# Performance work log

Measured on AMD Instinct MI355X. Metric: run time of the kernel, lower is better.

Reference implementation:

```python
import jax, jax.numpy as jnp
import numpy as np

B, Q, K, H = 4, 512, 512, 256

def setup_inputs() -> dict:
    key = jax.random.key(0)
    ks = jax.random.split(key, 6)
    scale = 1.0 / np.sqrt(H)
    return {
        "queries": jax.random.normal(ks[0], (B, Q, H), dtype=jnp.float32),
        "keys": jax.random.normal(ks[1], (B, K, H), dtype=jnp.float32),
        "values": jax.random.normal(ks[2], (B, K, H), dtype=jnp.float32),
        "W_q": jax.random.normal(ks[3], (H, H), dtype=jnp.float32) * scale,
        "W_k": jax.random.normal(ks[4], (H, H), dtype=jnp.float32) * scale,
        "w_v": jax.random.normal(ks[5], (H,), dtype=jnp.float32) * scale,
    }

def reference(queries, keys, values, W_q, W_k, w_v):
    # Linear (no bias): x @ W.T, matching torch nn.Linear convention
    q = jnp.einsum('bqh,oh->bqo', queries, W_q)      # [B,Q,H]
    k = jnp.einsum('bkh,oh->bko', keys, W_k)          # [B,K,H]
    # broadcast add -> tanh -> linear reduce to scores [B,Q,K]
    features = jnp.tanh(q[:, :, None, :] + k[:, None, :, :])  # [B,Q,K,H]
    scores = jnp.einsum('bqkh,h->bqk', features, w_v)          # [B,Q,K]
    attn = jax.nn.softmax(scores, axis=-1)                     # [B,Q,K]
    # dropout p=0 (eval) -> identity
    return jnp.einsum('bqk,bkd->bqd', attn, values)            # [B,Q,Dv]
```

## Files before the change

kernel.cpp:

```cpp
#include <hip/hip_runtime.h>
#include <hip/hip_bf16.h>
#include <math.h>


#define B_ 4
#define Q_ 512
#define K_ 512
#define H_ 256

#define QE_ELEMS (B_ * Q_ * H_)
#define KE_ELEMS (B_ * H_ * K_)
#define HALF_ELEMS (QE_ELEMS + KE_ELEMS)

static constexpr float CEXP = 2.8853900817779268f;
static constexpr float LOG2E = 1.4426950408889634f;

__global__ __launch_bounds__(256) void proj_partial(
    const float* __restrict__ queries, const float* __restrict__ keys,
    const float* __restrict__ Wq, const float* __restrict__ Wk,
    float* __restrict__ ws)
{
    const int bid = blockIdx.x;
    const float* A; const float* S; float* Cp; int ldc;
    if (bid < 256) {
        int dhalf = bid & 1;
        int tile = bid >> 1;
        int mt = tile >> 2, nt = tile & 3;
        A = queries + (mt * 64) * H_ + dhalf * 128;
        S = Wq + (nt * 64) * H_ + dhalf * 128;
        Cp = ws + (long)dhalf * HALF_ELEMS + (mt * 64) * H_ + nt * 64;
        ldc = H_;
    } else {
        int id = bid - 256;
        int dhalf = id & 1;
        int tile = id >> 1;
        int b = tile >> 5, mt = (tile >> 3) & 3, nt = tile & 7;
        A = Wk + (mt * 64) * H_ + dhalf * 128;
        S = keys + ((long)b * K_ + nt * 64) * H_ + dhalf * 128;
        Cp = ws + (long)dhalf * HALF_ELEMS + QE_ELEMS +
             ((long)b * H_ + mt * 64) * K_ + nt * 64;
        ldc = K_;
    }

    __shared__ float As[2][16][68];
    __shared__ float Ss[2][16][68];

    const int tid = threadIdx.x;
    const int tx = tid & 15;
    const int ty = tid >> 4;
    const int ldr = tid >> 2;
    const int ldd = (tid & 3) * 4;

    const float* GA = A + ldr * H_ + ldd;
    const float* GS = S + ldr * H_ + ldd;

    float4 av = *(const float4*)GA;
    float4 sv = *(const float4*)GS;
    As[0][ldd + 0][ldr] = av.x; As[0][ldd + 1][ldr] = av.y;
    As[0][ldd + 2][ldr] = av.z; As[0][ldd + 3][ldr] = av.w;
    Ss[0][ldd + 0][ldr] = sv.x; Ss[0][ldd + 1][ldr] = sv.y;
    Ss[0][ldd + 2][ldr] = sv.z; Ss[0][ldd + 3][ldr] = sv.w;

    float acc[4][4] = {};

#pragma unroll
    for (int c = 0; c < 8; ++c) {
        const int cur = c & 1;
        if (c < 7) {
            av = *(const float4*)(GA + (c + 1) * 16);
            sv = *(const float4*)(GS + (c + 1) * 16);
        }
        __syncthreads();
#pragma unroll
        for (int dd = 0; dd < 16; ++dd) {
            float4 a4 = *(const float4*)&As[cur][dd][ty * 4];
            float4 b4 = *(const float4*)&Ss[cur][dd][tx * 4];
            float am[4] = {a4.x, a4.y, a4.z, a4.w};
            float bn[4] = {b4.x, b4.y, b4.z, b4.w};
#pragma unroll
            for (int i = 0; i < 4; ++i)
#pragma unroll
                for (int j = 0; j < 4; ++j)
                    acc[i][j] = fmaf(am[i], bn[j], acc[i][j]);
        }
        if (c < 7) {
            const int nxt = cur ^ 1;
            As[nxt][ldd + 0][ldr] = av.x; As[nxt][ldd + 1][ldr] = av.y;
            As[nxt][ldd + 2][ldr] = av.z; As[nxt][ldd + 3][ldr] = av.w;
            Ss[nxt][ldd + 0][ldr] = sv.x; Ss[nxt][ldd + 1][ldr] = sv.y;
            Ss[nxt][ldd + 2][ldr] = sv.z; Ss[nxt][ldd + 3][ldr] = sv.w;
        }
    }

#pragma unroll
    for (int i = 0; i < 4; ++i) {
        float4 o = {acc[i][0], acc[i][1], acc[i][2], acc[i][3]};
        *(float4*)&Cp[(ty * 4 + i) * ldc + tx * 4] = o;
    }
}

__global__ __launch_bounds__(256) void exp_combine(float* __restrict__ ws)
{
    const int i = blockIdx.x * 256 + threadIdx.x;
    float4* w4 = (float4*)ws;
    float4 a = w4[i];
    float4 b = w4[i + HALF_ELEMS / 4];
    float4 o;
    o.x = __builtin_amdgcn_exp2f(CEXP * (a.x + b.x));
    o.y = __builtin_amdgcn_exp2f(CEXP * (a.y + b.y));
    o.z = __builtin_amdgcn_exp2f(CEXP * (a.z + b.z));
    o.w = __builtin_amdgcn_exp2f(CEXP * (a.w + b.w));
    w4[i] = o;
}

__global__ __launch_bounds__(1024, 8) void attn_fused(
    const float* __restrict__ qe, const float* __restrict__ ke,
    const float* __restrict__ values, const float* __restrict__ wv,
    float* __restrict__ out)
{
    const int b = blockIdx.y;
    const int q0 = blockIdx.x * 4;
    const int t = threadIdx.x;

    __shared__ __align__(16) float smem[4 * H_ + H_ + 4 * K_ + 4 * K_];
    float* sQ  = smem;
    float* wvs = smem + 4 * H_;
    float* sS  = smem + 5 * H_;
    float* sP  = smem + 5 * H_ + 4 * K_;

    sQ[t & 1023] = qe[((long)(b * Q_ + q0 + (t >> 8))) * H_ + (t & 255)];
    if (t < H_) wvs[t] = wv[t];
    __syncthreads();

    {
        const int k = t & 511;
        const int hh = t >> 9;
        const float* keb = ke + ((long)b * H_ + hh * 128) * K_ + k;

        float n0 = keb[0 * K_], n1 = keb[1 * K_], n2 = keb[2 * K_], n3 = keb[3 * K_];
        float acc[4] = {0.f, 0.f, 0.f, 0.f};

#pragma unroll 2
        for (int hl = 0; hl < 128; hl += 4) {
            float k0 = n0, k1 = n1, k2 = n2, k3 = n3;
            if (hl < 124) {
                const float* p = keb + (hl + 4) * K_;
                n0 = p[0]; n1 = p[K_]; n2 = p[2 * K_]; n3 = p[3 * K_];
            }
            const int h = hh * 128 + hl;
            float4 w4 = *(const float4*)&wvs[h];
#pragma unroll
            for (int q = 0; q < 4; ++q) {
                float4 e = *(const float4*)&sQ[q * H_ + h];
                float t0 = fmaf(e.x, k0, 1.0f);
                float t1 = fmaf(e.y, k1, 1.0f);
                float t2 = fmaf(e.z, k2, 1.0f);
                float t3 = fmaf(e.w, k3, 1.0f);
                float d01 = t0 * t1, d23 = t2 * t3;
                float n01 = fmaf(w4.x, t1, w4.y * t0);
                float n23 = fmaf(w4.z, t3, w4.w * t2);
                float num = fmaf(n01, d23, n23 * d01);
                acc[q] = fmaf(num, __builtin_amdgcn_rcpf(d01 * d23), acc[q]);
            }
        }

        if (hh == 1) {
#pragma unroll
            for (int q = 0; q < 4; ++q) sP[q * K_ + k] = acc[q];
        }
        __syncthreads();
        if (hh == 0) {
#pragma unroll
            for (int q = 0; q < 4; ++q)
                sS[q * K_ + k] = -2.0f * (acc[q] + sP[q * K_ + k]);
        }
    }
    __syncthreads();

    if (t < 256) {
        const int lane = t & 63;
        const int q = t >> 6;
        float sv[8];
        float m = -INFINITY;
#pragma unroll
        for (int j = 0; j < 8; ++j) {
            sv[j] = sS[q * K_ + lane + 64 * j];
            m = fmaxf(m, sv[j]);
        }
#pragma unroll
        for (int off = 32; off >= 1; off >>= 1) m = fmaxf(m, __shfl_xor(m, off));
        float sum = 0.f;
#pragma unroll
        for (int j = 0; j < 8; ++j) {
            sv[j] = __builtin_amdgcn_exp2f((sv[j] - m) * LOG2E);
            sum += sv[j];
        }
#pragma unroll
        for (int off = 32; off >= 1; off >>= 1) sum += __shfl_xor(sum, off);
        float rs = 1.0f / sum;
#pragma unroll
        for (int j = 0; j < 8; ++j) sS[q * K_ + lane + 64 * j] = sv[j] * rs;
    }
    __syncthreads();

    {
        const int lane = t & 63;
        const int h4 = lane * 4;
        const int q = (t >> 6) & 3;
        const int kq = t >> 8;
        const float* vb = values + (long)b * K_ * H_ + h4;
        const float* sSq = sS + q * K_;
        float4 acc = {0.f, 0.f, 0.f, 0.f};
        const int kbeg = kq * 128;
        for (int k = kbeg; k < kbeg + 128; k += 4) {
            float4 a = *(const float4*)&sSq[k];
            float4 v0 = *(const float4*)&vb[(k + 0) * H_];
            float4 v1 = *(const float4*)&vb[(k + 1) * H_];
            float4 v2 = *(const float4*)&vb[(k + 2) * H_];
            float4 v3 = *(const float4*)&vb[(k + 3) * H_];
            acc.x = fmaf(a.x, v0.x, fmaf(a.y, v1.x, fmaf(a.z, v2.x, fmaf(a.w, v3.x, acc.x))));
            acc.y = fmaf(a.x, v0.y, fmaf(a.y, v1.y, fmaf(a.z, v2.y, fmaf(a.w, v3.y, acc.y))));
            acc.z = fmaf(a.x, v0.z, fmaf(a.y, v1.z, fmaf(a.z, v2.z, fmaf(a.w, v3.z, acc.z))));
            acc.w = fmaf(a.x, v0.w, fmaf(a.y, v1.w, fmaf(a.z, v2.w, fmaf(a.w, v3.w, acc.w))));
        }
        __syncthreads();
        float4* sRed = (float4*)sS;
        if (kq) sRed[(kq - 1) * 256 + q * 64 + lane] = acc;
        __syncthreads();
        if (kq == 0) {
            float4 p1 = sRed[q * 64 + lane];
            float4 p2 = sRed[256 + q * 64 + lane];
            float4 p3 = sRed[512 + q * 64 + lane];
            acc.x += p1.x + p2.x + p3.x;
            acc.y += p1.y + p2.y + p3.y;
            acc.z += p1.z + p2.z + p3.z;
            acc.w += p1.w + p2.w + p3.w;
            *(float4*)&out[((long)(b * Q_ + q0 + q)) * H_ + h4] = acc;
        }
    }
}

extern "C" void kernel_launch(void* const* d_in, const int* in_sizes, int n_in,
                              void* d_out, int out_size, void* d_ws, size_t ws_size,
                              hipStream_t stream) {
    const float* queries = (const float*)d_in[0];
    const float* keys    = (const float*)d_in[1];
    const float* values  = (const float*)d_in[2];
    const float* Wq      = (const float*)d_in[3];
    const float* Wk      = (const float*)d_in[4];
    const float* wv      = (const float*)d_in[5];
    float* out = (float*)d_out;

    float* ws = (float*)d_ws;
    float* qe = ws;
    float* ke = ws + QE_ELEMS;

    proj_partial<<<512, 256, 0, stream>>>(queries, keys, Wq, Wk, ws);
    exp_combine<<<HALF_ELEMS / 1024, 256, 0, stream>>>(ws);
    attn_fused<<<dim3(Q_ / 4, B_), 1024, 0, stream>>>(qe, ke, values, wv, out);
}
```

Baseline: 137.5 us.

## Fuse projection, exp and attention into one persistent kernel with grid barrier

Merges the three launches into a single 512-block kernel. Each block first computes one projection tile, with two 256-thread teams splitting the reduction dimension and combining through LDS before applying the exp, then all blocks meet at an atomic grid barrier before the attention phase. This removes two kernel launches and the partial-sum round trip through global memory, and remaps attention blocks so batches follow XCD assignment. The trade-offs are that half the threads sit idle during the GEMM phase, and the grid barrier relies on all 512 blocks being co-resident, which would deadlock otherwise. It also adds a memset launch, double-buffers the key prefetch and unrolls the values loop.

New measurement: 318.1 us. +131.4%, slower.

```diff
diff --git a/kernel.cpp b/kernel.cpp
--- a/kernel.cpp
+++ b/kernel.cpp
@@ -7,162 +7,216 @@
 #define Q_ 512
 #define K_ 512
 #define H_ 256
-
 #define QE_ELEMS (B_ * Q_ * H_)
 #define KE_ELEMS (B_ * H_ * K_)
-#define HALF_ELEMS (QE_ELEMS + KE_ELEMS)
 
 static constexpr float CEXP = 2.8853900817779268f;
 static constexpr float LOG2E = 1.4426950408889634f;
 
-__global__ __launch_bounds__(256) void proj_partial(
+union Arena {
+    struct {
+        float As[2][2][16][68];
+        float Ss[2][2][16][68];
+    } ga;
+    struct {
+        float sQ[4 * H_];
+        float wvs[H_];
+        float sS[4 * K_];
+        float sP[4 * K_];
+    } at;
+};
+
+__device__ inline void grid_barrier(unsigned* ctr, unsigned expected) {
+    __syncthreads();
+    if (threadIdx.x == 0) {
+        __threadfence();
+        __hip_atomic_fetch_add(ctr, 1u, __ATOMIC_RELEASE,
+                               __HIP_MEMORY_SCOPE_AGENT);
+        while (__hip_atomic_load(ctr, __ATOMIC_ACQUIRE,
+                                 __HIP_MEMORY_SCOPE_AGENT) < expected)
+            __builtin_amdgcn_s_sleep(2);
+    }
+    __syncthreads();
+}
+
+__global__ __launch_bounds__(1024, 8) void fused_all(
     const float* __restrict__ queries, const float* __restrict__ keys,
-    const float* __restrict__ Wq, const float* __restrict__ Wk,
-    float* __restrict__ ws)
+    const float* __restrict__ values, const float* __restrict__ Wq,
+    const float* __restrict__ Wk, const float* __restrict__ wv,
+    float* __restrict__ ws, float* __restrict__ out,
+    unsigned* __restrict__ ctr)
 {
+    __shared__ Arena u;
     const int bid = blockIdx.x;
-    const float* A; const float* S; float* Cp; int ldc;
+    const int t = threadIdx.x;
+    float* qe = ws;
+    float* ke = ws + QE_ELEMS;
+
     if (bid < 256) {
-        int dhalf = bid & 1;
-        int tile = bid >> 1;
-        int mt = tile >> 2, nt = tile & 3;
-        A = queries + (mt * 64) * H_ + dhalf * 128;
-        S = Wq + (nt * 64) * H_ + dhalf * 128;
-        Cp = ws + (long)dhalf * HALF_ELEMS + (mt * 64) * H_ + nt * 64;
-        ldc = H_;
-    } else {
-        int id = bid - 256;
-        int dhalf = id & 1;
-        int tile = id >> 1;
-        int b = tile >> 5, mt = (tile >> 3) & 3, nt = tile & 7;
-        A = Wk + (mt * 64) * H_ + dhalf * 128;
-        S = keys + ((long)b * K_ + nt * 64) * H_ + dhalf * 128;
-        Cp = ws + (long)dhalf * HALF_ELEMS + QE_ELEMS +
-             ((long)b * H_ + mt * 64) * K_ + nt * 64;
-        ldc = K_;
-    }
-
-    __shared__ float As[2][16][68];
-    __shared__ float Ss[2][16][68];
-
-    const int tid = threadIdx.x;
-    const int tx = tid & 15;
-    const int ty = tid >> 4;
-    const int ldr = tid >> 2;
-    const int ldd = (tid & 3) * 4;
-
-    const float* GA = A + ldr * H_ + ldd;
-    const float* GS = S + ldr * H_ + ldd;
-
-    float4 av = *(const float4*)GA;
-    float4 sv = *(const float4*)GS;
-    As[0][ldd + 0][ldr] = av.x; As[0][ldd + 1][ldr] = av.y;
-    As[0][ldd + 2][ldr] = av.z; As[0][ldd + 3][ldr] = av.w;
-    Ss[0][ldd + 0][ldr] = sv.x; Ss[0][ldd + 1][ldr] = sv.y;
-    Ss[0][ldd + 2][ldr] = sv.z; Ss[0][ldd + 3][ldr] = sv.w;
-
-    float acc[4][4] = {};
-
-#pragma unroll
-    for (int c = 0; c < 8; ++c) {
-        const int cur = c & 1;
-        if (c < 7) {
-            av = *(const float4*)(GA + (c + 1) * 16);
-            sv = *(const float4*)(GS + (c + 1) * 16);
-        }
-        __syncthreads();
-#pragma unroll
-        for (int dd = 0; dd < 16; ++dd) {
-            float4 a4 = *(const float4*)&As[cur][dd][ty * 4];
-            float4 b4 = *(const float4*)&Ss[cur][dd][tx * 4];
-            float am[4] = {a4.x, a4.y, a4.z, a4.w};
-            float bn[4] = {b4.x, b4.y, b4.z, b4.w};
-#pragma unroll
-            for (int i = 0; i < 4; ++i)
-#pragma unroll
-                for (int j = 0; j < 4; ++j)
-                    acc[i][j] = fmaf(am[i], bn[j], acc[i][j]);
-        }
-        if (c < 7) {
-            const int nxt = cur ^ 1;
-            As[nxt][ldd + 0][ldr] = av.x; As[nxt][ldd + 1][ldr] = av.y;
-            As[nxt][ldd + 2][ldr] = av.z; As[nxt][ldd + 3][ldr] = av.w;
-            Ss[nxt][ldd + 0][ldr] = sv.x; Ss[nxt][ldd + 1][ldr] = sv.y;
-            Ss[nxt][ldd + 2][ldr] = sv.z; Ss[nxt][ldd + 3][ldr] = sv.w;
-        }
-    }
-
-#pragma unroll
-    for (int i = 0; i < 4; ++i) {
-        float4 o = {acc[i][0], acc[i][1], acc[i][2], acc[i][3]};
-        *(float4*)&Cp[(ty * 4 + i) * ldc + tx * 4] = o;
-    }
-}
-
-__global__ __launch_bounds__(256) void exp_combine(float* __restrict__ ws)
-{
-    const int i = blockIdx.x * 256 + threadIdx.x;
-    float4* w4 = (float4*)ws;
-    float4 a = w4[i];
-    float4 b = w4[i + HALF_ELEMS / 4];
-    float4 o;
-    o.x = __builtin_amdgcn_exp2f(CEXP * (a.x + b.x));
-    o.y = __builtin_amdgcn_exp2f(CEXP * (a.y + b.y));
-    o.z = __builtin_amdgcn_exp2f(CEXP * (a.z + b.z));
-    o.w = __builtin_amdgcn_exp2f(CEXP * (a.w + b.w));
-    w4[i] = o;
-}
-
-__global__ __launch_bounds__(1024, 8) void attn_fused(
-    const float* __restrict__ qe, const float* __restrict__ ke,
-    const float* __restrict__ values, const float* __restrict__ wv,
-    float* __restrict__ out)
-{
-    const int b = blockIdx.y;
-    const int q0 = blockIdx.x * 4;
-    const int t = threadIdx.x;
-
-    __shared__ __align__(16) float smem[4 * H_ + H_ + 4 * K_ + 4 * K_];
-    float* sQ  = smem;
-    float* wvs = smem + 4 * H_;
-    float* sS  = smem + 5 * H_;
-    float* sP  = smem + 5 * H_ + 4 * K_;
-
-    sQ[t & 1023] = qe[((long)(b * Q_ + q0 + (t >> 8))) * H_ + (t & 255)];
+        const int team = t >> 8;
+        const int tid = t & 255;
+        const bool active = team < 2;
+        const int dh = team & 1;
+
+        const float* A; const float* S; float* C; int ldc;
+        if (bid < 128) {
+            int mt = bid >> 2, nt = bid & 3;
+            A = queries + (mt * 64) * H_ + dh * 128;
+            S = Wq + (nt * 64) * H_ + dh * 128;
+            C = qe + (mt * 64) * H_ + nt * 64;
+            ldc = H_;
+        } else {
+            int id = bid - 128;
+            int b = id >> 5, mt = (id >> 3) & 3, nt = id & 7;
+            A = Wk + (mt * 64) * H_ + dh * 128;
+            S = keys + ((long)(b * K_ + nt * 64)) * H_ + dh * 128;
+            C = ke + ((long)(b * H_ + mt * 64)) * K_ + nt * 64;
+            ldc = K_;
+        }
+
+        const int tx = tid & 15;
+        const int ty = tid >> 4;
+        const int ldr = tid >> 2;
+        const int ldd = (tid & 3) * 4;
+        const float* GA = A + ldr * H_ + ldd;
+        const float* GS = S + ldr * H_ + ldd;
+
+        float4 av = {0, 0, 0, 0}, sv = {0, 0, 0, 0};
+        if (active) {
+            av = *(const float4*)GA;
+            sv = *(const float4*)GS;
+            u.ga.As[team][0][ldd + 0][ldr] = av.x;
+            u.ga.As[team][0][ldd + 1][ldr] = av.y;
+            u.ga.As[team][0][ldd + 2][ldr] = av.z;
+            u.ga.As[team][0][ldd + 3][ldr] = av.w;
+            u.ga.Ss[team][0][ldd + 0][ldr] = sv.x;
+            u.ga.Ss[team][0][ldd + 1][ldr] = sv.y;
+            u.ga.Ss[team][0][ldd + 2][ldr] = sv.z;
+            u.ga.Ss[team][0][ldd + 3][ldr] = sv.w;
+        }
+
+        float acc[4][4] = {};
+#pragma unroll
+        for (int c = 0; c < 8; ++c) {
+            const int cur = c & 1;
+            if (active && c < 7) {
+                av = *(const float4*)(GA + (c + 1) * 16);
+                sv = *(const float4*)(GS + (c + 1) * 16);
+            }
+            __syncthreads();
+            if (active) {
+#pragma unroll
+                for (int dd = 0; dd < 16; ++dd) {
+                    float4 a4 = *(const float4*)&u.ga.As[team][cur][dd][ty * 4];
+                    float4 b4 = *(const float4*)&u.ga.Ss[team][cur][dd][tx * 4];
+                    float am[4] = {a4.x, a4.y, a4.z, a4.w};
+                    float bn[4] = {b4.x, b4.y, b4.z, b4.w};
+#pragma unroll
+                    for (int i = 0; i < 4; ++i)
+#pragma unroll
+                        for (int j = 0; j < 4; ++j)
+                            acc[i][j] = fmaf(am[i], bn[j], acc[i][j]);
+                }
+                if (c < 7) {
+                    const int nxt = cur ^ 1;
+                    u.ga.As[team][nxt][ldd + 0][ldr] = av.x;
+                    u.ga.As[team][nxt][ldd + 1][ldr] = av.y;
+                    u.ga.As[team][nxt][ldd + 2][ldr] = av.z;
+                    u.ga.As[team][nxt][ldd + 3][ldr] = av.w;
+                    u.ga.Ss[team][nxt][ldd + 0][ldr] = sv.x;
+                    u.ga.Ss[team][nxt][ldd + 1][ldr] = sv.y;
+                    u.ga.Ss[team][nxt][ldd + 2][ldr] = sv.z;
+                    u.ga.Ss[team][nxt][ldd + 3][ldr] = sv.w;
+                }
+            }
+        }
+
+        __syncthreads();
+        float (*Cmb)[68] = (float(*)[68]) & u.ga.As[0][0][0][0];
+        if (team == 1) {
+#pragma unroll
+            for (int i = 0; i < 4; ++i) {
+                float4 o = {acc[i][0], acc[i][1], acc[i][2], acc[i][3]};
+                *(float4*)&Cmb[ty * 4 + i][tx * 4] = o;
+            }
+        }
+        __syncthreads();
+        if (team == 0) {
+#pragma unroll
+            for (int i = 0; i < 4; ++i) {
+                float4 p = *(const float4*)&Cmb[ty * 4 + i][tx * 4];
+                float4 o;
+                o.x = __builtin_amdgcn_exp2f(CEXP * (acc[i][0] + p.x));
+                o.y = __builtin_amdgcn_exp2f(CEXP * (acc[i][1] + p.y));
+                o.z = __builtin_amdgcn_exp2f(CEXP * (acc[i][2] + p.z));
+                o.w = __builtin_amdgcn_exp2f(CEXP * (acc[i][3] + p.w));
+                *(float4*)&C[(ty * 4 + i) * ldc + tx * 4] = o;
+            }
+        }
+    }
+
+    grid_barrier(ctr, (unsigned)gridDim.x);
+
+    const int xcd = bid & 7;
+    const int b = xcd >> 1;
+    const int qt = ((bid >> 3) << 1) | (xcd & 1);
+    const int q0 = qt * 4;
+
+    float* sQ = u.at.sQ;
+    float* wvs = u.at.wvs;
+    float* sS = u.at.sS;
+    float* sP = u.at.sP;
+
+    sQ[t] = qe[((long)(b * Q_ + q0 + (t >> 8))) * H_ + (t & 255)];
     if (t < H_) wvs[t] = wv[t];
     __syncthreads();
 
     {
         const int k = t & 511;
         const int hh = t >> 9;
-        const float* keb = ke + ((long)b * H_ + hh * 128) * K_ + k;
-
-        float n0 = keb[0 * K_], n1 = keb[1 * K_], n2 = keb[2 * K_], n3 = keb[3 * K_];
+        const float* keb = ke + ((long)(b * H_ + hh * 128)) * K_ + k;
+
+        float p0[4], p1[4];
+#pragma unroll
+        for (int j = 0; j < 4; ++j) p0[j] = keb[j * K_];
+#pragma unroll
+        for (int j = 0; j < 4; ++j) p1[j] = keb[(4 + j) * K_];
         float acc[4] = {0.f, 0.f, 0.f, 0.f};
 
-#pragma unroll 2
-        for (int hl = 0; hl < 128; hl += 4) {
-            float k0 = n0, k1 = n1, k2 = n2, k3 = n3;
-            if (hl < 124) {
-                const float* p = keb + (hl + 4) * K_;
-                n0 = p[0]; n1 = p[K_]; n2 = p[2 * K_]; n3 = p[3 * K_];
-            }
-            const int h = hh * 128 + hl;
-            float4 w4 = *(const float4*)&wvs[h];
-#pragma unroll
-            for (int q = 0; q < 4; ++q) {
-                float4 e = *(const float4*)&sQ[q * H_ + h];
-                float t0 = fmaf(e.x, k0, 1.0f);
-                float t1 = fmaf(e.y, k1, 1.0f);
-                float t2 = fmaf(e.z, k2, 1.0f);
-                float t3 = fmaf(e.w, k3, 1.0f);
-                float d01 = t0 * t1, d23 = t2 * t3;
-                float n01 = fmaf(w4.x, t1, w4.y * t0);
-                float n23 = fmaf(w4.z, t3, w4.w * t2);
-                float num = fmaf(n01, d23, n23 * d01);
-                acc[q] = fmaf(num, __builtin_amdgcn_rcpf(d01 * d23), acc[q]);
-            }
-        }
+#define QUAD(HB, K0, K1, K2, K3)                                          \
+        {                                                                 \
+            float4 w4 = *(const float4*)&wvs[HB];                         \
+            _Pragma("unroll")                                             \
+            for (int q = 0; q < 4; ++q) {                                 \
+                float4 e = *(const float4*)&sQ[q * H_ + (HB)];            \
+                float t0 = fmaf(e.x, K0, 1.0f);                           \
+                float t1 = fmaf(e.y, K1, 1.0f);                           \
+                float t2 = fmaf(e.z, K2, 1.0f);                           \
+                float t3 = fmaf(e.w, K3, 1.0f);                           \
+                float d01 = t0 * t1, d23 = t2 * t3;                       \
+                float n01 = fmaf(w4.x, t1, w4.y * t0);                    \
+                float n23 = fmaf(w4.z, t3, w4.w * t2);                    \
+                float num = fmaf(n01, d23, n23 * d01);                    \
+                acc[q] = fmaf(num, __builtin_amdgcn_rcpf(d01 * d23),      \
+                              acc[q]);                                    \
+            }                                                             \
+        }
+
+        for (int hl = 0; hl < 128; hl += 8) {
+            float k0 = p0[0], k1 = p0[1], k2 = p0[2], k3 = p0[3];
+            if (hl < 120) {
+                const float* p = keb + (hl + 8) * K_;
+                p0[0] = p[0]; p0[1] = p[K_]; p0[2] = p[2 * K_]; p0[3] = p[3 * K_];
+            }
+            QUAD(hh * 128 + hl, k0, k1, k2, k3)
+            float m0 = p1[0], m1 = p1[1], m2 = p1[2], m3 = p1[3];
+            if (hl < 120) {
+                const float* p = keb + (hl + 12) * K_;
+                p1[0] = p[0]; p1[1] = p[K_]; p1[2] = p[2 * K_]; p1[3] = p[3 * K_];
+            }
+            QUAD(hh * 128 + hl + 4, m0, m1, m2, m3)
+        }
+#undef QUAD
 
         if (hh == 1) {
 #pragma unroll
@@ -212,6 +266,7 @@
         const float* sSq = sS + q * K_;
         float4 acc = {0.f, 0.f, 0.f, 0.f};
         const int kbeg = kq * 128;
+#pragma unroll 2
         for (int k = kbeg; k < kbeg + 128; k += 4) {
             float4 a = *(const float4*)&sSq[k];
             float4 v0 = *(const float4*)&vb[(k + 0) * H_];
@@ -252,10 +307,9 @@
     float* out = (float*)d_out;
 
     float* ws = (float*)d_ws;
-    float* qe = ws;
-    float* ke = ws + QE_ELEMS;
-
-    proj_partial<<<512, 256, 0, stream>>>(queries, keys, Wq, Wk, ws);
-    exp_combine<<<HALF_ELEMS / 1024, 256, 0, stream>>>(ws);
-    attn_fused<<<dim3(Q_ / 4, B_), 1024, 0, stream>>>(qe, ke, values, wv, out);
+    unsigned* ctr = (unsigned*)(ws + QE_ELEMS + KE_ELEMS);
+
+    hipMemsetAsync((void*)ctr, 0, sizeof(unsigned), stream);
+    fused_all<<<512, 1024, 0, stream>>>(queries, keys, values, Wq, Wk, wv,
+                                        ws, out, ctr);
 }
```

## Fuse projection split-K reduction with exp into one kernel; remap attention blocks

Applied to the files above, without the earlier changes.

The projection kernel now uses 1024-thread blocks with four teams, each handling a quarter of the H reduction. The partial sums are reduced through shared memory and the exp is applied in the epilogue, so the separate exp_combine kernel and its global round-trip of partial sums are gone. The attention kernel splits the H dimension across four groups with two keys per thread instead of two groups with one key. Its grid is flattened and remapped so blocks of the same batch land on the same XCDs, aiming for better L2 reuse of ke and values. The trade-offs are a larger shared-memory reduction, fewer projection blocks (256 with 1024 threads), and more register pressure in the score loop.

After: 134.1 us. 2.5% less time.

```diff
diff --git a/kernel.cpp b/kernel.cpp
--- a/kernel.cpp
+++ b/kernel.cpp
@@ -7,74 +7,69 @@
 #define Q_ 512
 #define K_ 512
 #define H_ 256
-
 #define QE_ELEMS (B_ * Q_ * H_)
 #define KE_ELEMS (B_ * H_ * K_)
-#define HALF_ELEMS (QE_ELEMS + KE_ELEMS)
 
 static constexpr float CEXP = 2.8853900817779268f;
 static constexpr float LOG2E = 1.4426950408889634f;
 
-__global__ __launch_bounds__(256) void proj_partial(
+#define PJ_AS(team, buf, dd, row) smem[(((team)*2 + (buf)) * 16 + (dd)) * 68 + (row)]
+#define PJ_SS(team, buf, dd, row) smem[8704 + (((team)*2 + (buf)) * 16 + (dd)) * 68 + (row)]
+
+__global__ __launch_bounds__(1024, 4) void proj_exp(
     const float* __restrict__ queries, const float* __restrict__ keys,
     const float* __restrict__ Wq, const float* __restrict__ Wk,
-    float* __restrict__ ws)
+    float* __restrict__ qe, float* __restrict__ ke)
 {
+    __shared__ __align__(16) float smem[17408];
+
     const int bid = blockIdx.x;
-    const float* A; const float* S; float* Cp; int ldc;
-    if (bid < 256) {
-        int dhalf = bid & 1;
-        int tile = bid >> 1;
-        int mt = tile >> 2, nt = tile & 3;
-        A = queries + (mt * 64) * H_ + dhalf * 128;
-        S = Wq + (nt * 64) * H_ + dhalf * 128;
-        Cp = ws + (long)dhalf * HALF_ELEMS + (mt * 64) * H_ + nt * 64;
+    const int team = threadIdx.x >> 8;
+    const int tid = threadIdx.x & 255;
+
+    const float* A; const float* S; float* C; int ldc;
+    if (bid < 128) {
+        int mt = bid >> 2, nt = bid & 3;
+        A = queries + (mt * 64) * H_;
+        S = Wq + (nt * 64) * H_;
+        C = qe + (mt * 64) * H_ + nt * 64;
         ldc = H_;
     } else {
-        int id = bid - 256;
-        int dhalf = id & 1;
-        int tile = id >> 1;
-        int b = tile >> 5, mt = (tile >> 3) & 3, nt = tile & 7;
-        A = Wk + (mt * 64) * H_ + dhalf * 128;
-        S = keys + ((long)b * K_ + nt * 64) * H_ + dhalf * 128;
-        Cp = ws + (long)dhalf * HALF_ELEMS + QE_ELEMS +
-             ((long)b * H_ + mt * 64) * K_ + nt * 64;
+        int id = bid - 128;
+        int b = id >> 5, mt = (id >> 3) & 3, nt = id & 7;
+        A = Wk + (mt * 64) * H_;
+        S = keys + ((long)(b * K_ + nt * 64)) * H_;
+        C = ke + ((long)(b * H_ + mt * 64)) * K_ + nt * 64;
         ldc = K_;
     }
 
-    __shared__ float As[2][16][68];
-    __shared__ float Ss[2][16][68];
-
-    const int tid = threadIdx.x;
     const int tx = tid & 15;
     const int ty = tid >> 4;
     const int ldr = tid >> 2;
     const int ldd = (tid & 3) * 4;
-
-    const float* GA = A + ldr * H_ + ldd;
-    const float* GS = S + ldr * H_ + ldd;
+    const float* GA = A + ldr * H_ + team * 64 + ldd;
+    const float* GS = S + ldr * H_ + team * 64 + ldd;
 
     float4 av = *(const float4*)GA;
     float4 sv = *(const float4*)GS;
-    As[0][ldd + 0][ldr] = av.x; As[0][ldd + 1][ldr] = av.y;
-    As[0][ldd + 2][ldr] = av.z; As[0][ldd + 3][ldr] = av.w;
-    Ss[0][ldd + 0][ldr] = sv.x; Ss[0][ldd + 1][ldr] = sv.y;
-    Ss[0][ldd + 2][ldr] = sv.z; Ss[0][ldd + 3][ldr] = sv.w;
+    PJ_AS(team, 0, ldd + 0, ldr) = av.x; PJ_AS(team, 0, ldd + 1, ldr) = av.y;
+    PJ_AS(team, 0, ldd + 2, ldr) = av.z; PJ_AS(team, 0, ldd + 3, ldr) = av.w;
+    PJ_SS(team, 0, ldd + 0, ldr) = sv.x; PJ_SS(team, 0, ldd + 1, ldr) = sv.y;
+    PJ_SS(team, 0, ldd + 2, ldr) = sv.z; PJ_SS(team, 0, ldd + 3, ldr) = sv.w;
 
     float acc[4][4] = {};
-
-#pragma unroll
-    for (int c = 0; c < 8; ++c) {
+#pragma unroll
+    for (int c = 0; c < 4; ++c) {
         const int cur = c & 1;
-        if (c < 7) {
+        if (c < 3) {
             av = *(const float4*)(GA + (c + 1) * 16);
             sv = *(const float4*)(GS + (c + 1) * 16);
         }
         __syncthreads();
 #pragma unroll
         for (int dd = 0; dd < 16; ++dd) {
-            float4 a4 = *(const float4*)&As[cur][dd][ty * 4];
-            float4 b4 = *(const float4*)&Ss[cur][dd][tx * 4];
+            float4 a4 = *(const float4*)&PJ_AS(team, cur, dd, ty * 4);
+            float4 b4 = *(const float4*)&PJ_SS(team, cur, dd, tx * 4);
             float am[4] = {a4.x, a4.y, a4.z, a4.w};
             float bn[4] = {b4.x, b4.y, b4.z, b4.w};
 #pragma unroll
@@ -83,96 +78,140 @@
                 for (int j = 0; j < 4; ++j)
                     acc[i][j] = fmaf(am[i], bn[j], acc[i][j]);
         }
-        if (c < 7) {
+        if (c < 3) {
             const int nxt = cur ^ 1;
-            As[nxt][ldd + 0][ldr] = av.x; As[nxt][ldd + 1][ldr] = av.y;
-            As[nxt][ldd + 2][ldr] = av.z; As[nxt][ldd + 3][ldr] = av.w;
-            Ss[nxt][ldd + 0][ldr] = sv.x; Ss[nxt][ldd + 1][ldr] = sv.y;
-            Ss[nxt][ldd + 2][ldr] = sv.z; Ss[nxt][ldd + 3][ldr] = sv.w;
-        }
-    }
-
-#pragma unroll
-    for (int i = 0; i < 4; ++i) {
-        float4 o = {acc[i][0], acc[i][1], acc[i][2], acc[i][3]};
-        *(float4*)&Cp[(ty * 4 + i) * ldc + tx * 4] = o;
+            PJ_AS(team, nxt, ldd + 0, ldr) = av.x;
+            PJ_AS(team, nxt, ldd + 1, ldr) = av.y;
+            PJ_AS(team, nxt, ldd + 2, ldr) = av.z;
+            PJ_AS(team, nxt, ldd + 3, ldr) = av.w;
+            PJ_SS(team, nxt, ldd + 0, ldr) = sv.x;
+            PJ_SS(team, nxt, ldd + 1, ldr) = sv.y;
+            PJ_SS(team, nxt, ldd + 2, ldr) = sv.z;
+            PJ_SS(team, nxt, ldd + 3, ldr) = sv.w;
+        }
+    }
+
+    __syncthreads();
+    if (team > 0) {
+        float* Cmb = smem + (team - 1) * 4352;
+#pragma unroll
+        for (int i = 0; i < 4; ++i) {
+            float4 o = {acc[i][0], acc[i][1], acc[i][2], acc[i][3]};
+            *(float4*)&Cmb[(ty * 4 + i) * 68 + tx * 4] = o;
+        }
+    }
+    __syncthreads();
+    if (team == 0) {
+#pragma unroll
+        for (int i = 0; i < 4; ++i) {
+            const int off = (ty * 4 + i) * 68 + tx * 4;
+            float4 p1 = *(const float4*)&smem[off];
+            float4 p2 = *(const float4*)&smem[4352 + off];
+            float4 p3 = *(const float4*)&smem[8704 + off];
+            float4 o;
+            o.x = __builtin_amdgcn_exp2f(CEXP * (acc[i][0] + p1.x + p2.x + p3.x));
+            o.y = __builtin_amdgcn_exp2f(CEXP * (acc[i][1] + p1.y + p2.y + p3.y));
+            o.z = __builtin_amdgcn_exp2f(CEXP * (acc[i][2] + p1.z + p2.z + p3.z));
+            o.w = __builtin_amdgcn_exp2f(CEXP * (acc[i][3] + p1.w + p2.w + p3.w));
+            *(float4*)&C[(ty * 4 + i) * ldc + tx * 4] = o;
+        }
     }
 }
 
-__global__ __launch_bounds__(256) void exp_combine(float* __restrict__ ws)
-{
-    const int i = blockIdx.x * 256 + threadIdx.x;
-    float4* w4 = (float4*)ws;
-    float4 a = w4[i];
-    float4 b = w4[i + HALF_ELEMS / 4];
-    float4 o;
-    o.x = __builtin_amdgcn_exp2f(CEXP * (a.x + b.x));
-    o.y = __builtin_amdgcn_exp2f(CEXP * (a.y + b.y));
-    o.z = __builtin_amdgcn_exp2f(CEXP * (a.z + b.z));
-    o.w = __builtin_amdgcn_exp2f(CEXP * (a.w + b.w));
-    w4[i] = o;
-}
-
-__global__ __launch_bounds__(1024, 8) void attn_fused(
+__global__ __launch_bounds__(1024, 8) void attn(
     const float* __restrict__ qe, const float* __restrict__ ke,
     const float* __restrict__ values, const float* __restrict__ wv,
     float* __restrict__ out)
 {
-    const int b = blockIdx.y;
-    const int q0 = blockIdx.x * 4;
+    const int bid = blockIdx.x;
+    const int xcd = bid & 7;
+    const int b = xcd >> 1;
+    const int q0 = (((bid >> 3) << 1) | (xcd & 1)) * 4;
     const int t = threadIdx.x;
 
-    __shared__ __align__(16) float smem[4 * H_ + H_ + 4 * K_ + 4 * K_];
+    __shared__ __align__(16) float smem[9472];
     float* sQ  = smem;
     float* wvs = smem + 4 * H_;
     float* sS  = smem + 5 * H_;
     float* sP  = smem + 5 * H_ + 4 * K_;
 
-    sQ[t & 1023] = qe[((long)(b * Q_ + q0 + (t >> 8))) * H_ + (t & 255)];
+    sQ[t] = qe[((long)(b * Q_ + q0 + (t >> 8))) * H_ + (t & 255)];
     if (t < H_) wvs[t] = wv[t];
     __syncthreads();
 
     {
-        const int k = t & 511;
-        const int hh = t >> 9;
-        const float* keb = ke + ((long)b * H_ + hh * 128) * K_ + k;
-
-        float n0 = keb[0 * K_], n1 = keb[1 * K_], n2 = keb[2 * K_], n3 = keb[3 * K_];
-        float acc[4] = {0.f, 0.f, 0.f, 0.f};
-
-#pragma unroll 2
-        for (int hl = 0; hl < 128; hl += 4) {
-            float k0 = n0, k1 = n1, k2 = n2, k3 = n3;
-            if (hl < 124) {
+        const int k = t & 255;
+        const int g = t >> 8;
+        const float* keb = ke + ((long)(b * H_ + g * 64)) * K_ + k;
+
+        float nx[8];
+#pragma unroll
+        for (int j = 0; j < 4; ++j) {
+            nx[2 * j + 0] = keb[j * K_];
+            nx[2 * j + 1] = keb[j * K_ + 256];
+        }
+        float acc[4][2] = {};
+
+        for (int hl = 0; hl < 64; hl += 4) {
+            float c0 = nx[0], c1 = nx[1], c2 = nx[2], c3 = nx[3];
+            float c4 = nx[4], c5 = nx[5], c6 = nx[6], c7 = nx[7];
+            if (hl < 60) {
                 const float* p = keb + (hl + 4) * K_;
-                n0 = p[0]; n1 = p[K_]; n2 = p[2 * K_]; n3 = p[3 * K_];
+                nx[0] = p[0];        nx[1] = p[256];
+                nx[2] = p[K_];       nx[3] = p[K_ + 256];
+                nx[4] = p[2 * K_];   nx[5] = p[2 * K_ + 256];
+                nx[6] = p[3 * K_];   nx[7] = p[3 * K_ + 256];
             }
-            const int h = hh * 128 + hl;
+            const int h = g * 64 + hl;
             float4 w4 = *(const float4*)&wvs[h];
 #pragma unroll
             for (int q = 0; q < 4; ++q) {
                 float4 e = *(const float4*)&sQ[q * H_ + h];
-                float t0 = fmaf(e.x, k0, 1.0f);
-                float t1 = fmaf(e.y, k1, 1.0f);
-                float t2 = fmaf(e.z, k2, 1.0f);
-                float t3 = fmaf(e.w, k3, 1.0f);
-                float d01 = t0 * t1, d23 = t2 * t3;
-                float n01 = fmaf(w4.x, t1, w4.y * t0);
-                float n23 = fmaf(w4.z, t3, w4.w * t2);
-                float num = fmaf(n01, d23, n23 * d01);
-                acc[q] = fmaf(num, __builtin_amdgcn_rcpf(d01 * d23), acc[q]);
+                {
+                    float t0 = fmaf(e.x, c0, 1.0f);
+                    float t1 = fmaf(e.y, c2, 1.0f);
+                    float t2 = fmaf(e.z, c4, 1.0f);
+                    float t3 = fmaf(e.w, c6, 1.0f);
+                    float d01 = t0 * t1, d23 = t2 * t3;
+                    float n01 = fmaf(w4.x, t1, w4.y * t0);
+                    float n23 = fmaf(w4.z, t3, w4.w * t2);
+                    float num = fmaf(n01, d23, n23 * d01);
+                    acc[q][0] = fmaf(num, __builtin_amdgcn_rcpf(d01 * d23), acc[q][0]);
+                }
+                {
+                    float t0 = fmaf(e.x, c1, 1.0f);
+                    float t1 = fmaf(e.y, c3, 1.0f);
+                    float t2 = fmaf(e.z, c5, 1.0f);
+                    float t3 = fmaf(e.w, c7, 1.0f);
+                    float d01 = t0 * t1, d23 = t2 * t3;
+                    float n01 = fmaf(w4.x, t1, w4.y * t0);
+                    float n23 = fmaf(w4.z, t3, w4.w * t2);
+                    float num = fmaf(n01, d23, n23 * d01);
+                    acc[q][1] = fmaf(num, __builtin_amdgcn_rcpf(d01 * d23), acc[q][1]);
+                }
             }
         }
 
-        if (hh == 1) {
-#pragma unroll
-            for (int q = 0; q < 4; ++q) sP[q * K_ + k] = acc[q];
-        }
-        __syncthreads();
-        if (hh == 0) {
+        if (g > 0) {
+            float* dst = sP + (g - 1) * 4 * K_;
+#pragma unroll
+            for (int q = 0; q < 4; ++q) {
+                dst[q * K_ + k] = acc[q][0];
+                dst[q * K_ + k + 256] = acc[q][1];
+            }
+        }
+        __syncthreads();
+        if (g == 0) {
 #pragma unroll
             for (int q = 0; q < 4; ++q)
-                sS[q * K_ + k] = -2.0f * (acc[q] + sP[q * K_ + k]);
+#pragma unroll
+                for (int kk = 0; kk < 2; ++kk) {
+                    const int kc = k + kk * 256;
+                    float s = acc[q][kk] + sP[0 * 4 * K_ + q * K_ + kc]
+                            + sP[1 * 4 * K_ + q * K_ + kc]
+                            + sP[2 * 4 * K_ + q * K_ + kc];
+                    sS[q * K_ + kc] = -2.0f * s;
+                }
         }
     }
     __syncthreads();
@@ -212,6 +251,7 @@
         const float* sSq = sS + q * K_;
         float4 acc = {0.f, 0.f, 0.f, 0.f};
         const int kbeg = kq * 128;
+#pragma unroll 2
         for (int k = kbeg; k < kbeg + 128; k += 4) {
             float4 a = *(const float4*)&sSq[k];
             float4 v0 = *(const float4*)&vb[(k + 0) * H_];
@@ -251,11 +291,9 @@
     const float* wv      = (const float*)d_in[5];
     float* out = (float*)d_out;
 
-    float* ws = (float*)d_ws;
-    float* qe = ws;
-    float* ke = ws + QE_ELEMS;
-
-    proj_partial<<<512, 256, 0, stream>>>(queries, keys, Wq, Wk, ws);
-    exp_combine<<<HALF_ELEMS / 1024, 256, 0, stream>>>(ws);
-    attn_fused<<<dim3(Q_ / 4, B_), 1024, 0, stream>>>(qe, ke, values, wv, out);
+    float* qe = (float*)d_ws;
+    float* ke = qe + QE_ELEMS;
+
+    proj_exp<<<256, 1024, 0, stream>>>(queries, keys, Wq, Wk, qe, ke);
+    attn<<<512, 1024, 0, stream>>>(qe, ke, values, wv, out);
 }
```
